# Performance work log

Measured on AMD Instinct MI355X. Metric: run time of the kernel, lower is better.

## Reference

```python
import jax, jax.numpy as jnp
import numpy as np


def setup_inputs() -> dict:
    key = jax.random.key(0)
    kx, kq, kk, kv = jax.random.split(key, 4)
    d_model, d_head = 1024, 64
    x = jax.random.normal(kx, (4, 4096, d_model), dtype=jnp.float32)
    scale = 1.0 / np.sqrt(d_model)
    Wq = jax.random.normal(kq, (d_model, d_head), dtype=jnp.float32) * scale
    Wk = jax.random.normal(kk, (d_model, d_head), dtype=jnp.float32) * scale
    Wv = jax.random.normal(kv, (d_model, d_head), dtype=jnp.float32) * scale
    return {"x": x, "Wq": Wq, "Wk": Wk, "Wv": Wv}


def reference(x, Wq, Wk, Wv):
    # x: [B, S, D]; Wq/Wk/Wv: [D, H]
    d_head = Wq.shape[-1]
    Q = jnp.einsum('bsd,dh->bsh', x, Wq)
    K = jnp.einsum('bsd,dh->bsh', x, Wk)
    V = jnp.einsum('bsd,dh->bsh', x, Wv)
    scores = jnp.einsum('bqh,bkh->bqk', Q, K) / jnp.sqrt(jnp.float32(d_head))
    S = x.shape[1]
    causal = jnp.tril(jnp.ones((S, S), dtype=bool))  # [S, S]
    scores = jnp.where(causal, scores, -jnp.inf)
    weights = jax.nn.softmax(scores, axis=-1)  # [B, S, S]
    return jnp.einsum('bqk,bkh->bqh', weights, V)
```

## Files before the change

### kernel.cpp

```cpp
#include <hip/hip_runtime.h>

#define D_MODEL 1024
#define D_HEAD  64
#define SEQ     4096
#define BATCH   4
#define M_TOT   (BATCH * SEQ)
#define LOG2E   1.44269504088896f
#define MFIX_L2 17.3123404906676f
#define CHUNK   4

typedef __bf16 bf16;
typedef bf16  bf16x8 __attribute__((ext_vector_type(8)));
typedef float f32x4  __attribute__((ext_vector_type(4)));

#define MFMA(a, b, c) __builtin_amdgcn_mfma_f32_16x16x32_bf16(a, b, c, 0, 0, 0)

#define QKV_OFF 0
#define OBUF_OFF 6291456
#define LBUF_OFF 10485760
#define WT_OFF   10551296

__global__ void prep_kernel(const float* __restrict__ Wq, const float* __restrict__ Wk,
                            const float* __restrict__ Wv, bf16* __restrict__ Wt,
                            float4* __restrict__ zp, int n4)
{
    const int bx = blockIdx.x;
    const int t  = threadIdx.x;
    if (bx < 48) {
        __shared__ bf16 tr[64][72];
        const int wm = bx >> 4, kt = bx & 15, k0 = kt * 64;
        const float* W = (wm == 0) ? Wq : (wm == 1) ? Wk : Wv;
        const int kr = t >> 2, nb = (t & 3) * 16;
        #pragma unroll
        for (int j = 0; j < 4; j++) {
            float4 wrow = *(const float4*)(W + (size_t)(k0 + kr) * D_HEAD + nb + j * 4);
            tr[nb + j * 4 + 0][kr] = (bf16)wrow.x;
            tr[nb + j * 4 + 1][kr] = (bf16)wrow.y;
            tr[nb + j * 4 + 2][kr] = (bf16)wrow.z;
            tr[nb + j * 4 + 3][kr] = (bf16)wrow.w;
        }
        __syncthreads();
        const int n = t >> 2, kc = (t & 3) * 8;
        bf16* dst = Wt + (size_t)(wm * 64 + n) * D_MODEL + k0;
        #pragma unroll
        for (int h = 0; h < 2; h++) {
            bf16x8 v;
            #pragma unroll
            for (int j = 0; j < 8; j++) v[j] = tr[n][kc + h * 32 + j];
            *(bf16x8*)(dst + kc + h * 32) = v;
        }
    } else {
        int i = (bx - 48) * 256 + t;
        if (i < n4) zp[i] = float4{0.f, 0.f, 0.f, 0.f};
    }
}

#define XP 40

__global__ __launch_bounds__(512) void proj_kernel(
    const float* __restrict__ x, const bf16* __restrict__ Wt,
    bf16* __restrict__ qkv)
{
    __shared__ __align__(16) bf16 xs[2][64][XP];
    __shared__ __align__(16) bf16 ws[2][192][XP];
    __shared__ float red[64][193];

    const int t    = threadIdx.x;
    const int w    = t >> 6;
    const int g    = w >> 2;
    const int nw   = w & 3;
    const int lane = t & 63;
    const int quad = lane >> 4;
    const int l15  = lane & 15;
    const int row0 = blockIdx.x * 64;
    const int kb   = g * 512;

    const int tg   = t & 255;
    const int xrow = tg >> 2, xkq = (tg & 3) * 8;

    const float* xg = x + (size_t)(row0 + xrow) * D_MODEL + kb + xkq;

    f32x4 acc[12] = {};

    float4 xa = *(const float4*)(xg);
    float4 xb = *(const float4*)(xg + 4);
    bf16x8 wtv[3];
    #pragma unroll
    for (int it = 0; it < 3; it++) {
        int id = tg + it * 256, n = id >> 2, kk8 = (id & 3) * 8;
        wtv[it] = *(const bf16x8*)(Wt + (size_t)n * D_MODEL + kb + kk8);
    }

    for (int k0 = 0; k0 < 512; k0 += 32) {
        bf16x8 xv;
        xv[0] = (bf16)xa.x; xv[1] = (bf16)xa.y; xv[2] = (bf16)xa.z; xv[3] = (bf16)xa.w;
        xv[4] = (bf16)xb.x; xv[5] = (bf16)xb.y; xv[6] = (bf16)xb.z; xv[7] = (bf16)xb.w;
        *(bf16x8*)&xs[g][xrow][xkq] = xv;
        #pragma unroll
        for (int it = 0; it < 3; it++) {
            int id = tg + it * 256, n = id >> 2, kk8 = (id & 3) * 8;
            *(bf16x8*)&ws[g][n][kk8] = wtv[it];
        }
        __syncthreads();

        const int k1 = k0 + 32;
        if (k1 < 512) {
            xa = *(const float4*)(xg + k1);
            xb = *(const float4*)(xg + k1 + 4);
            #pragma unroll
            for (int it = 0; it < 3; it++) {
                int id = tg + it * 256, n = id >> 2, kk8 = (id & 3) * 8;
                wtv[it] = *(const bf16x8*)(Wt + (size_t)n * D_MODEL + kb + k1 + kk8);
            }
        }

        bf16x8 af[4], bfr[3];
        #pragma unroll
        for (int rg = 0; rg < 4; rg++)
            af[rg] = *(bf16x8*)&xs[g][rg * 16 + l15][quad * 8];
        #pragma unroll
        for (int j = 0; j < 3; j++)
            bfr[j] = *(bf16x8*)&ws[g][nw * 48 + j * 16 + l15][quad * 8];
        #pragma unroll
        for (int rg = 0; rg < 4; rg++)
            #pragma unroll
            for (int j = 0; j < 3; j++)
                acc[rg * 3 + j] = MFMA(af[rg], bfr[j], acc[rg * 3 + j]);
        __syncthreads();
    }

    if (g == 1) {
        #pragma unroll
        for (int rg = 0; rg < 4; rg++)
            #pragma unroll
            for (int j = 0; j < 3; j++)
                #pragma unroll
                for (int r = 0; r < 4; r++)
                    red[rg * 16 + quad * 4 + r][nw * 48 + j * 16 + l15] =
                        acc[rg * 3 + j][r];
    }
    __syncthreads();
    if (g == 0) {
        #pragma unroll
        for (int rg = 0; rg < 4; rg++)
            #pragma unroll
            for (int j = 0; j < 3; j++) {
                const int col = nw * 48 + j * 16 + l15;
                const int wm = col >> 6, h = col & 63;
                const float sc = (wm == 0) ? 0.125f : 1.0f;
                bf16* outp = qkv + (size_t)wm * M_TOT * D_HEAD;
                #pragma unroll
                for (int r = 0; r < 4; r++) {
                    const int row = rg * 16 + quad * 4 + r;
                    float s = acc[rg * 3 + j][r] + red[row][col];
                    outp[(size_t)(row0 + row) * D_HEAD + h] = (bf16)(s * sc);
                }
            }
    }
}

#define TS 72

__global__ __launch_bounds__(256) void attn_kernel(
    const bf16* __restrict__ qkv, float* __restrict__ o_buf,
    float* __restrict__ l_buf)
{
    const int i = blockIdx.x;
    const int c = blockIdx.y;
    const int b = blockIdx.z;
    const int ntiles = i + 1;
    const int tile0  = c * CHUNK;
    if (tile0 >= ntiles) return;
    const int tile1 = min(tile0 + CHUNK, ntiles);

    __shared__ __align__(16) bf16 Ks[64][TS];
    __shared__ __align__(16) bf16 Vs[64][TS];
    __shared__ __align__(16) bf16 Ps[4][16][TS];

    const bf16* Q = qkv;
    const bf16* K = qkv + (size_t)M_TOT * D_HEAD;
    const bf16* V = qkv + (size_t)2 * M_TOT * D_HEAD;

    const int t    = threadIdx.x;
    const int wv   = t >> 6;
    const int lane = t & 63;
    const int quad = lane >> 4;
    const int l15  = lane & 15;
    const int qb   = i * 64;
    const size_t base = (size_t)b * SEQ * D_HEAD;

    bf16x8 qf0, qf1;
    {
        const bf16* qr = Q + base + (size_t)(qb + wv * 16 + l15) * D_HEAD;
        qf0 = *(const bf16x8*)(qr + quad * 8);
        qf1 = *(const bf16x8*)(qr + 32 + quad * 8);
    }

    f32x4 o[4] = {};
    float l_r[4] = {};
    const int qw0 = qb + wv * 16;

    const int krow = t >> 2;
    const int kq8  = (t & 3) * 8;
    const int vdim = t & 63;

    for (int tile = tile0; tile < tile1; tile++) {
        const int kk0 = tile * 64;
        {
            const bf16* kp = K + base + (size_t)(kk0 + krow) * D_HEAD;
            *(bf16x8*)&Ks[krow][kq8]      = *(const bf16x8*)(kp + kq8);
            *(bf16x8*)&Ks[krow][kq8 + 32] = *(const bf16x8*)(kp + kq8 + 32);
        }
        #pragma unroll
        for (int h = 0; h < 2; h++) {
            const int kk = (t >> 6) * 8 + h * 32;
            bf16x8 vvv;
            #pragma unroll
            for (int j = 0; j < 8; j++)
                vvv[j] = V[base + (size_t)(kk0 + kk + j) * D_HEAD + vdim];
            *(bf16x8*)&Vs[vdim][kk] = vvv;
        }
        __syncthreads();

        f32x4 sc4[4];
        #pragma unroll
        for (int kt = 0; kt < 4; kt++) {
            f32x4 z = {};
            z = MFMA(qf0, *(bf16x8*)&Ks[kt * 16 + l15][quad * 8],      z);
            z = MFMA(qf1, *(bf16x8*)&Ks[kt * 16 + l15][32 + quad * 8], z);
            sc4[kt] = z;
        }

        const bool need_mask = (tile == i);

        #pragma unroll
        for (int r = 0; r < 4; r++) {
            #pragma unroll
            for (int kt = 0; kt < 4; kt++) {
                float s = sc4[kt][r];
                if (need_mask && (kk0 + kt * 16 + l15 > qw0 + quad * 4 + r))
                    s = -1e30f;
                float p = __builtin_amdgcn_exp2f(fmaf(s, LOG2E, -MFIX_L2));
                l_r[r] += p;
                Ps[wv][quad * 4 + r][kt * 16 + l15] = (bf16)p;
            }
        }
        __syncthreads();

        #pragma unroll
        for (int c2 = 0; c2 < 2; c2++) {
            bf16x8 pa = *(bf16x8*)&Ps[wv][l15][c2 * 32 + quad * 8];
            #pragma unroll
            for (int t4 = 0; t4 < 4; t4++) {
                bf16x8 vb = *(bf16x8*)&Vs[t4 * 16 + l15][c2 * 32 + quad * 8];
                o[t4] = MFMA(pa, vb, o[t4]);
            }
        }
        __syncthreads();
    }

    const int mrow0 = b * SEQ + qw0;
    #pragma unroll
    for (int r = 0; r < 4; r++) {
        float ls = l_r[r];
        #pragma unroll
        for (int sh = 1; sh < 16; sh <<= 1)
            ls += __shfl_xor(ls, sh, 64);
        if (l15 == 0)
            atomicAdd(&l_buf[mrow0 + quad * 4 + r], ls);
        const size_t orow = (size_t)(mrow0 + quad * 4 + r) * D_HEAD;
        #pragma unroll
        for (int t4 = 0; t4 < 4; t4++)
            atomicAdd(&o_buf[orow + t4 * 16 + l15], o[t4][r]);
    }
}

__global__ void norm_kernel(const float4* __restrict__ o_buf,
                            const float* __restrict__ l_buf,
                            float4* __restrict__ out)
{
    int gid = blockIdx.x * 256 + threadIdx.x;
    int m = gid >> 4;
    float inv = 1.0f / l_buf[m];
    float4 v = o_buf[gid];
    out[gid] = float4{v.x * inv, v.y * inv, v.z * inv, v.w * inv};
}

extern "C" void kernel_launch(void* const* d_in, const int* in_sizes, int n_in,
                              void* d_out, int out_size, void* d_ws, size_t ws_size,
                              hipStream_t stream) {
    const float* x  = (const float*)d_in[0];
    const float* Wq = (const float*)d_in[1];
    const float* Wk = (const float*)d_in[2];
    const float* Wv = (const float*)d_in[3];

    bf16*  qkv   = (bf16*)((char*)d_ws + QKV_OFF);
    float* o_buf = (float*)((char*)d_ws + OBUF_OFF);
    float* l_buf = (float*)((char*)d_ws + LBUF_OFF);
    bf16*  Wt    = (bf16*)((char*)d_ws + WT_OFF);

    const int zero4 = (M_TOT * 65) / 4;
    const int zblocks = (zero4 + 255) / 256;
    prep_kernel<<<48 + zblocks, 256, 0, stream>>>(Wq, Wk, Wv, Wt,
                                                  (float4*)o_buf, zero4);
    proj_kernel<<<M_TOT / 64, 512, 0, stream>>>(x, Wt, qkv);
    attn_kernel<<<dim3(SEQ / 64, SEQ / 64 / CHUNK, BATCH), 256, 0, stream>>>(
        qkv, o_buf, l_buf);
    norm_kernel<<<M_TOT * 16 / 256, 256, 0, stream>>>((const float4*)o_buf, l_buf,
                                                      (float4*)d_out);
}
```

Before: 166.9 us.

## Double-buffer projection LDS, pre-transpose V, and prefetch K/V tiles in attention

The projection kernel now double-buffers its LDS tiles, so each chunk needs one barrier instead of two and the next tile is stored while the current one is consumed. A new kernel transposes V into a [B, H, S] layout. The attention kernel can then load V with vectorized loads instead of strided scalar gathers, and it prefetches the next K/V tile into registers during compute. The cost is an extra kernel launch and extra V traffic to global memory, plus doubled LDS use in proj_kernel, which may lower occupancy.

After: 160.6 us. -3.8%, faster.

```diff
diff --git a/kernel.cpp b/kernel.cpp
--- a/kernel.cpp
+++ b/kernel.cpp
@@ -15,10 +15,11 @@
 
 #define MFMA(a, b, c) __builtin_amdgcn_mfma_f32_16x16x32_bf16(a, b, c, 0, 0, 0)
 
-#define QKV_OFF 0
+#define QKV_OFF  0
 #define OBUF_OFF 6291456
 #define LBUF_OFF 10485760
 #define WT_OFF   10551296
+#define VT_OFF   10944512
 
 __global__ void prep_kernel(const float* __restrict__ Wq, const float* __restrict__ Wk,
                             const float* __restrict__ Wv, bf16* __restrict__ Wt,
@@ -61,8 +62,8 @@
     const float* __restrict__ x, const bf16* __restrict__ Wt,
     bf16* __restrict__ qkv)
 {
-    __shared__ __align__(16) bf16 xs[2][64][XP];
-    __shared__ __align__(16) bf16 ws[2][192][XP];
+    __shared__ __align__(16) bf16 xs[2][2][64][XP];
+    __shared__ __align__(16) bf16 ws[2][2][192][XP];
     __shared__ float red[64][193];
 
     const int t    = threadIdx.x;
@@ -82,51 +83,56 @@
 
     f32x4 acc[12] = {};
 
-    float4 xa = *(const float4*)(xg);
-    float4 xb = *(const float4*)(xg + 4);
+    float4 xa, xb;
     bf16x8 wtv[3];
-    #pragma unroll
-    for (int it = 0; it < 3; it++) {
-        int id = tg + it * 256, n = id >> 2, kk8 = (id & 3) * 8;
-        wtv[it] = *(const bf16x8*)(Wt + (size_t)n * D_MODEL + kb + kk8);
-    }
-
-    for (int k0 = 0; k0 < 512; k0 += 32) {
+
+    auto load_regs = [&](int c) {
+        xa = *(const float4*)(xg + c * 32);
+        xb = *(const float4*)(xg + c * 32 + 4);
+        #pragma unroll
+        for (int it = 0; it < 3; it++) {
+            int id = tg + it * 256, n = id >> 2, kk8 = (id & 3) * 8;
+            wtv[it] = *(const bf16x8*)(Wt + (size_t)n * D_MODEL + kb + c * 32 + kk8);
+        }
+    };
+    auto store_lds = [&](int p) {
         bf16x8 xv;
         xv[0] = (bf16)xa.x; xv[1] = (bf16)xa.y; xv[2] = (bf16)xa.z; xv[3] = (bf16)xa.w;
         xv[4] = (bf16)xb.x; xv[5] = (bf16)xb.y; xv[6] = (bf16)xb.z; xv[7] = (bf16)xb.w;
-        *(bf16x8*)&xs[g][xrow][xkq] = xv;
+        *(bf16x8*)&xs[p][g][xrow][xkq] = xv;
         #pragma unroll
         for (int it = 0; it < 3; it++) {
             int id = tg + it * 256, n = id >> 2, kk8 = (id & 3) * 8;
-            *(bf16x8*)&ws[g][n][kk8] = wtv[it];
-        }
-        __syncthreads();
-
-        const int k1 = k0 + 32;
-        if (k1 < 512) {
-            xa = *(const float4*)(xg + k1);
-            xb = *(const float4*)(xg + k1 + 4);
-            #pragma unroll
-            for (int it = 0; it < 3; it++) {
-                int id = tg + it * 256, n = id >> 2, kk8 = (id & 3) * 8;
-                wtv[it] = *(const bf16x8*)(Wt + (size_t)n * D_MODEL + kb + k1 + kk8);
-            }
-        }
-
+            *(bf16x8*)&ws[p][g][n][kk8] = wtv[it];
+        }
+    };
+
+    load_regs(0);
+    store_lds(0);
+    load_regs(1);
+    __syncthreads();
+
+    int p = 0;
+    for (int c = 0; c < 16; c++) {
         bf16x8 af[4], bfr[3];
         #pragma unroll
         for (int rg = 0; rg < 4; rg++)
-            af[rg] = *(bf16x8*)&xs[g][rg * 16 + l15][quad * 8];
+            af[rg] = *(bf16x8*)&xs[p][g][rg * 16 + l15][quad * 8];
         #pragma unroll
         for (int j = 0; j < 3; j++)
-            bfr[j] = *(bf16x8*)&ws[g][nw * 48 + j * 16 + l15][quad * 8];
+            bfr[j] = *(bf16x8*)&ws[p][g][nw * 48 + j * 16 + l15][quad * 8];
         #pragma unroll
         for (int rg = 0; rg < 4; rg++)
             #pragma unroll
             for (int j = 0; j < 3; j++)
                 acc[rg * 3 + j] = MFMA(af[rg], bfr[j], acc[rg * 3 + j]);
-        __syncthreads();
+
+        if (c + 1 < 16) {
+            store_lds(p ^ 1);
+            if (c + 2 < 16) load_regs(c + 2);
+        }
+        __syncthreads();
+        p ^= 1;
     }
 
     if (g == 1) {
@@ -159,11 +165,37 @@
     }
 }
 
+__global__ void vtrans_kernel(const bf16* __restrict__ qkv, bf16* __restrict__ vt)
+{
+    __shared__ bf16 trs[64][72];
+    const bf16* Vsec = qkv + (size_t)2 * M_TOT * D_HEAD;
+    const int t  = threadIdx.x;
+    const int m0 = blockIdx.x * 64;
+    const int b  = m0 >> 12, s0 = m0 & (SEQ - 1);
+
+    #pragma unroll
+    for (int half = 0; half < 2; half++) {
+        const int ml = (t >> 3) + half * 32, hc = t & 7;
+        bf16x8 v = *(const bf16x8*)(Vsec + (size_t)(m0 + ml) * D_HEAD + hc * 8);
+        #pragma unroll
+        for (int j = 0; j < 8; j++) trs[hc * 8 + j][ml] = v[j];
+    }
+    __syncthreads();
+    #pragma unroll
+    for (int half = 0; half < 2; half++) {
+        const int hl = (t >> 3) + half * 32, sc = t & 7;
+        bf16x8 v;
+        #pragma unroll
+        for (int j = 0; j < 8; j++) v[j] = trs[hl][sc * 8 + j];
+        *(bf16x8*)(vt + ((size_t)b * D_HEAD + hl) * SEQ + s0 + sc * 8) = v;
+    }
+}
+
 #define TS 72
 
 __global__ __launch_bounds__(256) void attn_kernel(
-    const bf16* __restrict__ qkv, float* __restrict__ o_buf,
-    float* __restrict__ l_buf)
+    const bf16* __restrict__ qkv, const bf16* __restrict__ vt,
+    float* __restrict__ o_buf, float* __restrict__ l_buf)
 {
     const int i = blockIdx.x;
     const int c = blockIdx.y;
@@ -179,7 +211,6 @@
 
     const bf16* Q = qkv;
     const bf16* K = qkv + (size_t)M_TOT * D_HEAD;
-    const bf16* V = qkv + (size_t)2 * M_TOT * D_HEAD;
 
     const int t    = threadIdx.x;
     const int wv   = t >> 6;
@@ -187,7 +218,8 @@
     const int quad = lane >> 4;
     const int l15  = lane & 15;
     const int qb   = i * 64;
-    const size_t base = (size_t)b * SEQ * D_HEAD;
+    const size_t base  = (size_t)b * SEQ * D_HEAD;
+    const bf16* vtb = vt + (size_t)b * D_HEAD * SEQ;
 
     bf16x8 qf0, qf1;
     {
@@ -200,27 +232,35 @@
     float l_r[4] = {};
     const int qw0 = qb + wv * 16;
 
-    const int krow = t >> 2;
-    const int kq8  = (t & 3) * 8;
-    const int vdim = t & 63;
+    const int dr  = t >> 2;
+    const int kq8 = (t & 3) * 8;
+
+    bf16x8 kr0, kr1, vr0, vr1;
+    {
+        const bf16* kp = K + base + (size_t)(tile0 * 64 + dr) * D_HEAD;
+        kr0 = *(const bf16x8*)(kp + kq8);
+        kr1 = *(const bf16x8*)(kp + kq8 + 32);
+        const bf16* vp = vtb + (size_t)dr * SEQ + tile0 * 64;
+        vr0 = *(const bf16x8*)(vp + kq8);
+        vr1 = *(const bf16x8*)(vp + kq8 + 32);
+    }
 
     for (int tile = tile0; tile < tile1; tile++) {
         const int kk0 = tile * 64;
-        {
-            const bf16* kp = K + base + (size_t)(kk0 + krow) * D_HEAD;
-            *(bf16x8*)&Ks[krow][kq8]      = *(const bf16x8*)(kp + kq8);
-            *(bf16x8*)&Ks[krow][kq8 + 32] = *(const bf16x8*)(kp + kq8 + 32);
-        }
-        #pragma unroll
-        for (int h = 0; h < 2; h++) {
-            const int kk = (t >> 6) * 8 + h * 32;
-            bf16x8 vvv;
-            #pragma unroll
-            for (int j = 0; j < 8; j++)
-                vvv[j] = V[base + (size_t)(kk0 + kk + j) * D_HEAD + vdim];
-            *(bf16x8*)&Vs[vdim][kk] = vvv;
-        }
-        __syncthreads();
+        *(bf16x8*)&Ks[dr][kq8]      = kr0;
+        *(bf16x8*)&Ks[dr][kq8 + 32] = kr1;
+        *(bf16x8*)&Vs[dr][kq8]      = vr0;
+        *(bf16x8*)&Vs[dr][kq8 + 32] = vr1;
+        __syncthreads();
+
+        if (tile + 1 < tile1) {
+            const bf16* kp = K + base + (size_t)((tile + 1) * 64 + dr) * D_HEAD;
+            kr0 = *(const bf16x8*)(kp + kq8);
+            kr1 = *(const bf16x8*)(kp + kq8 + 32);
+            const bf16* vp = vtb + (size_t)dr * SEQ + (tile + 1) * 64;
+            vr0 = *(const bf16x8*)(vp + kq8);
+            vr1 = *(const bf16x8*)(vp + kq8 + 32);
+        }
 
         f32x4 sc4[4];
         #pragma unroll
@@ -298,14 +338,16 @@
     float* o_buf = (float*)((char*)d_ws + OBUF_OFF);
     float* l_buf = (float*)((char*)d_ws + LBUF_OFF);
     bf16*  Wt    = (bf16*)((char*)d_ws + WT_OFF);
+    bf16*  vt    = (bf16*)((char*)d_ws + VT_OFF);
 
     const int zero4 = (M_TOT * 65) / 4;
     const int zblocks = (zero4 + 255) / 256;
     prep_kernel<<<48 + zblocks, 256, 0, stream>>>(Wq, Wk, Wv, Wt,
                                                   (float4*)o_buf, zero4);
     proj_kernel<<<M_TOT / 64, 512, 0, stream>>>(x, Wt, qkv);
+    vtrans_kernel<<<M_TOT / 64, 256, 0, stream>>>(qkv, vt);
     attn_kernel<<<dim3(SEQ / 64, SEQ / 64 / CHUNK, BATCH), 256, 0, stream>>>(
-        qkv, o_buf, l_buf);
+        qkv, vt, o_buf, l_buf);
     norm_kernel<<<M_TOT * 16 / 256, 256, 0, stream>>>((const float4*)o_buf, l_buf,
                                                       (float4*)d_out);
 }
```
